# Optimization experiments

Measured on AMD Instinct MI355X. Metric: run time of the kernel, lower is better.

The kernel has to match this reference:

```python
import jax, jax.numpy as jnp
import numpy as np

B, S, D, H, NL, V, E, DFF = 4, 512, 768, 12, 2, 32000, 8, 3072
CF = 1.25
HD = D // H


def setup_inputs() -> dict:
    key = jax.random.key(0)
    ks = jax.random.split(key, 12)
    r = lambda i, shape: jax.random.normal(ks[i], shape, jnp.float32) * 0.02
    return {
        "src": jax.random.randint(ks[0], (B, S), 0, V),
        "src_pad_mask": jnp.zeros((B, S), bool),
        "emb": r(1, (V, D)),
        "qkv_w": r(2, (NL, 3 * D, D)), "qkv_b": jnp.zeros((NL, 3 * D), jnp.float32),
        "out_w": r(3, (NL, D, D)), "out_b": jnp.zeros((NL, D), jnp.float32),
        "wr": r(4, (NL, D, E)),
        "w1": r(5, (NL, E, D, DFF)), "b1": jnp.zeros((NL, E, DFF), jnp.float32),
        "w2": r(6, (NL, E, DFF, D)), "b2": jnp.zeros((NL, E, D), jnp.float32),
        "ln1_g": jnp.ones((NL, D), jnp.float32), "ln1_b": jnp.zeros((NL, D), jnp.float32),
        "ln2_g": jnp.ones((NL, D), jnp.float32), "ln2_b": jnp.zeros((NL, D), jnp.float32),
        "lnf_g": jnp.ones((D,), jnp.float32), "lnf_b": jnp.zeros((D,), jnp.float32),
    }


def layernorm(x, g, b, eps=1e-5):
    mu = jnp.mean(x, -1, keepdims=True)
    var = jnp.mean((x - mu) ** 2, -1, keepdims=True)
    return (x - mu) * jax.lax.rsqrt(var + eps) * g + b


def pos_encoding():
    pos = jnp.arange(S, dtype=jnp.float32)[:, None]
    i = jnp.arange(0, D, 2, dtype=jnp.float32)
    ang = pos * jnp.exp(-(i / D) * jnp.log(jnp.float32(10000.0)))  # [S, D/2]
    pe = jnp.zeros((S, D), jnp.float32)
    pe = pe.at[:, 0::2].set(jnp.sin(ang)).at[:, 1::2].set(jnp.cos(ang))
    return pe


def mha(x, wqkv, bqkv, wo, bo, pad):
    qkv = x @ wqkv.T + bqkv
    q, k, v = jnp.split(qkv, 3, axis=-1)
    q = q.reshape(B, S, H, HD); k = k.reshape(B, S, H, HD); v = v.reshape(B, S, H, HD)
    sc = jnp.einsum('bqhd,bkhd->bhqk', q, k) * (1.0 / float(HD) ** 0.5)
    sc = jnp.where(pad[:, None, None, :], jnp.float32(-1e9), sc)
    at = jax.nn.softmax(sc, -1)
    o = jnp.einsum('bhqk,bkhd->bqhd', at, v).reshape(B, S, D)
    return o @ wo.T + bo


def switch_ffn(x, token_mask, wr, w1, b1, w2, b2):
    # Switch Transformer top-1 routing with capacity drop.
    T = B * S
    cap = int(CF * T / E)
    xf = x.reshape(T, D)
    vm = token_mask.reshape(T).astype(x.dtype)
    logits = xf @ wr                                   # [T, E]
    probs = jax.nn.softmax(logits, -1)
    idx = jnp.argmax(probs, -1)
    gate = jnp.take_along_axis(probs, idx[:, None], -1)[:, 0]
    oh = jax.nn.one_hot(idx, E, dtype=x.dtype) * vm[:, None]      # [T, E]
    pos = jnp.cumsum(oh, axis=0) * oh                  # 1-indexed position in expert
    keep = ((pos > 0) & (pos <= cap)).astype(x.dtype)
    disp = keep[:, :, None] * jax.nn.one_hot((pos - 1).astype(jnp.int32), cap, dtype=x.dtype)  # [T,E,C]
    comb = disp * gate[:, None, None]
    ein = jnp.einsum('tec,td->ecd', disp, xf)          # [E, C, D]
    hid = jax.nn.relu(jnp.einsum('ecd,edf->ecf', ein, w1) + b1[:, None, :])
    eo = jnp.einsum('ecf,efd->ecd', hid, w2) + b2[:, None, :]
    y = jnp.einsum('tec,ecd->td', comb, eo).reshape(B, S, D)
    denom = jnp.maximum(vm.sum(), 1.0)
    me = (probs * vm[:, None]).sum(0) / denom
    ce = oh.sum(0) / denom
    lb = jnp.float32(E) * jnp.sum(me * ce)
    z = jnp.sum((jax.nn.logsumexp(logits, -1) ** 2) * vm) / denom
    return y, lb, z


def forward(src, src_pad_mask, emb, qkv_w, qkv_b, out_w, out_b, wr, w1, b1, w2, b2,
            ln1_g, ln1_b, ln2_g, ln2_b, lnf_g, lnf_b):
    x = emb[src] * jnp.float32(float(D) ** 0.5) + pos_encoding()[None]
    token_mask = ~src_pad_mask
    lbs, zs = [], []
    for l in range(NL):
        xn = layernorm(x, ln1_g[l], ln1_b[l])
        x = x + mha(xn, qkv_w[l], qkv_b[l], out_w[l], out_b[l], src_pad_mask)
        xn = layernorm(x, ln2_g[l], ln2_b[l])
        y, lb, z = switch_ffn(xn, token_mask, wr[l], w1[l], b1[l], w2[l], b2[l])
        x = x + y
        lbs.append(lb); zs.append(z)
    x = layernorm(x, lnf_g, lnf_b)
    return x, jnp.stack(lbs).mean(), jnp.stack(zs).mean()


def reference(src, src_pad_mask, emb, qkv_w, qkv_b, out_w, out_b, wr, w1, b1, w2, b2,
              ln1_g, ln1_b, ln2_g, ln2_b, lnf_g, lnf_b):
    return forward(src, src_pad_mask, emb, qkv_w, qkv_b, out_w, out_b, wr, w1, b1, w2, b2,
                   ln1_g, ln1_b, ln2_g, ln2_b, lnf_g, lnf_b)
```

## Files before the change

### kernel.cpp

```cpp
#include <hip/hip_runtime.h>

#define BB 4
#define SS 512
#define DD 768
#define HH 12
#define NLAYER 2
#define EE 8
#define DFF 3072
#define TT 2048
#define CAP 320
#define HD 64

typedef unsigned short u16;
typedef long long ll;
typedef _Float16 f16x8 __attribute__((ext_vector_type(8)));
typedef float f32x4 __attribute__((ext_vector_type(4)));

union F16U { _Float16 h; u16 u; };

__device__ __forceinline__ void split2h(float v, u16& h0, u16& h1) {
    F16U c0; c0.h = (_Float16)v;
    float r = (v - (float)c0.h) * 4096.0f;
    F16U c1; c1.h = (_Float16)r;
    h0 = c0.u; h1 = c1.u;
}
__device__ __forceinline__ float rec2h(u16 a, u16 b) {
    F16U c0, c1; c0.u = a; c1.u = b;
    return (float)c0.h + (float)c1.h * (1.0f / 4096.0f);
}

#define MFMA16(a, b, c) __builtin_amdgcn_mfma_f32_16x16x32_f16(a, b, c, 0, 0, 0)

struct GemmP {
    const u16* A = nullptr; ll sAp = 0;
    const void* B = nullptr; ll sBp = 0;
    const float* bias = nullptr; ll biasStride = 0;
    void* C = nullptr; ll sCp = 0;
    int M = 0, N = 0, K = 0, lda = 0, ldb = 0, ldc = 0;
    int modA = 1; ll sA1 = 0, sA2 = 0;
    int modB = 1; ll sB1 = 0, sB2 = 0;
    int modC = 1; ll sC1 = 0, sC2 = 0;
    float alpha = 1.f;
    int flags = 0;
    int KS = 1; ll partStride = 0;
    int Jc = 1;
};

#define BK 64
#define PADK 72

template<bool BTRANS, int NS>
__global__ __launch_bounds__(256) void gemm_kernel(GemmP p) {
    __shared__ u16 Al[NS][128][PADK];
    __shared__ u16 Bl[NS][128][PADK];
    const int tid = threadIdx.x;

    int bx, by, bz;
    {
        int gx = gridDim.x, gy = gridDim.y;
        int NBt = gx * gy * gridDim.z;
        int L = blockIdx.x + gx * (blockIdx.y + gy * blockIdx.z);
        int q = NBt >> 3, r = NBt & 7;
        int xcd = L & 7, wi = L >> 3;
        int c = (xcd < r) ? xcd * (q + 1) + wi : r * (q + 1) + (xcd - r) * q + wi;
        int Jc = p.Jc;
        int gxJ = gx * Jc;
        int sj = c / gxJ;
        int t = c - sj * gxJ;
        bx = t / Jc;
        int j = sj * Jc + (t - (t / Jc) * Jc);
        by = j % gy; bz = j / gy;
    }
    const int n0 = bx * 128, m0 = by * 128;
    const int slice = bz % p.KS;
    const int z = bz / p.KS;
    const int kslice = p.K / p.KS;
    const int k0 = slice * kslice;
    const int nkt = kslice >> 6;

    const u16* Ap = p.A + (ll)(z % p.modA) * p.sA1 + (ll)(z / p.modA) * p.sA2 + k0;
    const ll zB = (ll)(z % p.modB) * p.sB1 + (ll)(z / p.modB) * p.sB2;
    const ll zC = (ll)(z % p.modC) * p.sC1 + (ll)(z / p.modC) * p.sC2;
    const u16* Bpu = BTRANS ? ((const u16*)p.B + zB + k0) : nullptr;
    const float* Bpf = BTRANS ? nullptr : ((const float*)p.B + zB);

    const int lane = tid & 63, wid = tid >> 6;
    const int wm = (wid >> 1) * 64, wn = (wid & 1) * 64;
    const int ar = lane & 15, kg = (lane >> 4) * 8;

    f32x4 acc0[4][4] = {};
    f32x4 acc1[4][4] = {};

    uint4 ra[4 * NS];
    uint4 rb[4 * NS];
    float rbf[32];

    auto loadA = [&](int kt) {
        #pragma unroll
        for (int s = 0; s < NS; ++s)
            #pragma unroll
            for (int h = 0; h < 4; ++h) {
                int c = tid + h * 256, row = c >> 3, q = c & 7;
                int gm = m0 + row;
                uint4 v = {0u, 0u, 0u, 0u};
                if (gm < p.M) v = *(const uint4*)(Ap + (ll)s * p.sAp + (size_t)gm * p.lda + kt * BK + q * 8);
                ra[s * 4 + h] = v;
            }
    };
    auto storeA = [&]() {
        #pragma unroll
        for (int s = 0; s < NS; ++s)
            #pragma unroll
            for (int h = 0; h < 4; ++h) {
                int c = tid + h * 256, row = c >> 3, q = c & 7;
                *(uint4*)&Al[s][row][q * 8] = ra[s * 4 + h];
            }
    };
    auto loadB = [&](int kt) {
        if (BTRANS) {
            #pragma unroll
            for (int s = 0; s < NS; ++s)
                #pragma unroll
                for (int h = 0; h < 4; ++h) {
                    int c = tid + h * 256, row = c >> 3, q = c & 7;
                    int gn = n0 + row;
                    uint4 v = {0u, 0u, 0u, 0u};
                    if (gn < p.N) v = *(const uint4*)(Bpu + (ll)s * p.sBp + (size_t)gn * p.ldb + kt * BK + q * 8);
                    rb[s * 4 + h] = v;
                }
        } else {
            int gn = n0 + (tid & 127);
            int kb = (tid >> 7) * 32;
            #pragma unroll
            for (int i = 0; i < 32; ++i) {
                float v = 0.f;
                if (gn < p.N) v = Bpf[(size_t)(k0 + kt * BK + kb + i) * p.ldb + gn];
                rbf[i] = v;
            }
        }
    };
    auto storeB = [&]() {
        if (BTRANS) {
            #pragma unroll
            for (int s = 0; s < NS; ++s)
                #pragma unroll
                for (int h = 0; h < 4; ++h) {
                    int c = tid + h * 256, row = c >> 3, q = c & 7;
                    *(uint4*)&Bl[s][row][q * 8] = rb[s * 4 + h];
                }
        } else {
            int col = tid & 127;
            int kb = (tid >> 7) * 32;
            #pragma unroll
            for (int i = 0; i < 8; ++i) {
                u16 t0[4], t1[4];
                #pragma unroll
                for (int e = 0; e < 4; ++e) split2h(rbf[i * 4 + e], t0[e], t1[e]);
                *(uint2*)&Bl[0][col][kb + i * 4] = *(uint2*)t0;
                if (NS == 2) *(uint2*)&Bl[1][col][kb + i * 4] = *(uint2*)t1;
            }
        }
    };

    loadA(0); loadB(0);
    for (int kt = 0; kt < nkt; ++kt) {
        storeA(); storeB();
        __syncthreads();
        if (kt + 1 < nkt) { loadA(kt + 1); loadB(kt + 1); }
        #pragma unroll
        for (int kt2 = 0; kt2 < 2; ++kt2) {
            f16x8 b0r[4], b1r[4];
            #pragma unroll
            for (int j = 0; j < 4; ++j) {
                b0r[j] = *(const f16x8*)&Bl[0][wn + j * 16 + ar][kt2 * 32 + kg];
                if (NS == 2) b1r[j] = *(const f16x8*)&Bl[1][wn + j * 16 + ar][kt2 * 32 + kg];
            }
            #pragma unroll
            for (int i = 0; i < 4; ++i) {
                f16x8 a0 = *(const f16x8*)&Al[0][wm + i * 16 + ar][kt2 * 32 + kg];
                f16x8 a1;
                if (NS == 2) a1 = *(const f16x8*)&Al[1][wm + i * 16 + ar][kt2 * 32 + kg];
                #pragma unroll
                for (int j = 0; j < 4; ++j) {
                    acc0[i][j] = MFMA16(a0, b0r[j], acc0[i][j]);
                    if (NS == 2) {
                        acc1[i][j] = MFMA16(a0, b1r[j], acc1[i][j]);
                        acc1[i][j] = MFMA16(a1, b0r[j], acc1[i][j]);
                    }
                }
            }
        }
        __syncthreads();
    }

    const bool doPart = (p.flags & 16);
    float* Cpart = doPart ? ((float*)p.C + (ll)slice * p.partStride + zC) : nullptr;
    const float* biasp = (p.flags & 1) ? (p.bias + (ll)z * p.biasStride) : nullptr;
    u16* C0 = (!doPart && (p.flags & 8)) ? ((u16*)p.C + zC) : nullptr;
    u16* C1 = C0 ? (C0 + p.sCp) : nullptr;
    float* Cf = (!doPart && !(p.flags & 8)) ? ((float*)p.C + zC) : nullptr;
    #pragma unroll
    for (int i = 0; i < 4; ++i) {
        #pragma unroll
        for (int j = 0; j < 4; ++j) {
            int gc = n0 + wn + j * 16 + (lane & 15);
            if (gc >= p.N) continue;
            int gr0 = m0 + wm + i * 16 + (lane >> 4) * 4;
            #pragma unroll
            for (int r = 0; r < 4; ++r) {
                int gr = gr0 + r;
                if (gr >= p.M) continue;
                float v = acc0[i][j][r];
                if (NS == 2) v += acc1[i][j][r] * (1.0f / 4096.0f);
                v *= p.alpha;
                size_t off = (size_t)gr * p.ldc + gc;
                if (doPart) { Cpart[off] = v; continue; }
                if (p.flags & 1) v = __fadd_rn(v, biasp[gc]);
                if (p.flags & 2) v = fmaxf(v, 0.f);
                if (p.flags & 8) { u16 h0, h1; split2h(v, h0, h1); C0[off] = h0; C1[off] = h1; }
                else Cf[off] = v;
            }
        }
    }
}

__global__ __launch_bounds__(256) void flash_kernel(
    const u16* __restrict__ qkvp, ll sQp,
    const u16* __restrict__ vTp, ll sVp,
    const unsigned char* __restrict__ pad,
    u16* __restrict__ attnp, ll sOp) {
    __shared__ u16 KV[2][64][72];
    __shared__ u16 Pl[2][4][16][72];

    int L = blockIdx.x;
    int c = (L & 7) * 48 + (L >> 3);
    int bh = c >> 3, qt = c & 7;
    int b = bh / HH, h = bh % HH;
    int lane = threadIdx.x & 63, wv = threadIdx.x >> 6;
    int qbase = b * SS + qt * 64 + wv * 16;

    int spl = threadIdx.x >> 7;
    int srr = threadIdx.x & 127;
    int srow = srr >> 1, shalf = srr & 1;

    f16x8 qf[2][2];
    {
        const u16* qr = qkvp + (size_t)(qbase + (lane & 15)) * (3 * DD) + h * HD + (lane >> 4) * 8;
        #pragma unroll
        for (int kt2 = 0; kt2 < 2; ++kt2)
            #pragma unroll
            for (int pl = 0; pl < 2; ++pl)
                qf[kt2][pl] = *(const f16x8*)(qr + (ll)pl * sQp + kt2 * 32);
    }

    f32x4 S[32];
    #pragma unroll
    for (int kv = 0; kv < 8; ++kv) {
        const u16* gk = qkvp + (size_t)(b * SS + kv * 64 + srow) * (3 * DD) + DD + h * HD + (ll)spl * sQp;
        #pragma unroll
        for (int qq = 0; qq < 4; ++qq) {
            int off = shalf * 32 + qq * 8;
            *(uint4*)&KV[spl][srow][off] = *(const uint4*)(gk + off);
        }
        __syncthreads();
        #pragma unroll
        for (int nf = 0; nf < 4; ++nf) {
            f32x4 a0 = {}, a1 = {};
            #pragma unroll
            for (int kt2 = 0; kt2 < 2; ++kt2) {
                f16x8 b0 = *(const f16x8*)&KV[0][nf * 16 + (lane & 15)][kt2 * 32 + (lane >> 4) * 8];
                f16x8 b1 = *(const f16x8*)&KV[1][nf * 16 + (lane & 15)][kt2 * 32 + (lane >> 4) * 8];
                a0 = MFMA16(qf[kt2][0], b0, a0);
                a1 = MFMA16(qf[kt2][0], b1, a1);
                a1 = MFMA16(qf[kt2][1], b0, a1);
            }
            int col = kv * 64 + nf * 16 + (lane & 15);
            bool msk = pad[b * SS + col] != 0;
            #pragma unroll
            for (int r = 0; r < 4; ++r) {
                float v = (a0[r] + a1[r] * (1.0f / 4096.0f)) * 0.125f;
                S[kv * 4 + nf][r] = msk ? -1e9f : v;
            }
        }
        __syncthreads();
    }

    float mx[4] = {-1e30f, -1e30f, -1e30f, -1e30f}, sm[4] = {0.f, 0.f, 0.f, 0.f}, inv[4];
    #pragma unroll
    for (int f = 0; f < 32; ++f)
        #pragma unroll
        for (int r = 0; r < 4; ++r) mx[r] = fmaxf(mx[r], S[f][r]);
    #pragma unroll
    for (int r = 0; r < 4; ++r) {
        #pragma unroll
        for (int off = 1; off < 16; off <<= 1) mx[r] = fmaxf(mx[r], __shfl_xor(mx[r], off));
    }
    #pragma unroll
    for (int f = 0; f < 32; ++f)
        #pragma unroll
        for (int r = 0; r < 4; ++r) { float e = expf(S[f][r] - mx[r]); S[f][r] = e; sm[r] += e; }
    #pragma unroll
    for (int r = 0; r < 4; ++r) {
        #pragma unroll
        for (int off = 1; off < 16; off <<= 1) sm[r] += __shfl_xor(sm[r], off);
        inv[r] = 1.f / sm[r];
    }

    f32x4 p0[4] = {}, p1[4] = {};
    #pragma unroll
    for (int kv = 0; kv < 8; ++kv) {
        const u16* gv = vTp + (size_t)bh * HD * SS + (size_t)srow * SS + kv * 64 + (ll)spl * sVp;
        #pragma unroll
        for (int qq = 0; qq < 4; ++qq) {
            int off = shalf * 32 + qq * 8;
            *(uint4*)&KV[spl][srow][off] = *(const uint4*)(gv + off);
        }
        #pragma unroll
        for (int nf = 0; nf < 4; ++nf)
            #pragma unroll
            for (int r = 0; r < 4; ++r) {
                float v = S[kv * 4 + nf][r] * inv[r];
                u16 h0, h1; split2h(v, h0, h1);
                Pl[0][wv][(lane >> 4) * 4 + r][nf * 16 + (lane & 15)] = h0;
                Pl[1][wv][(lane >> 4) * 4 + r][nf * 16 + (lane & 15)] = h1;
            }
        __syncthreads();
        f16x8 pa[2][2];
        #pragma unroll
        for (int kt2 = 0; kt2 < 2; ++kt2)
            #pragma unroll
            for (int pl = 0; pl < 2; ++pl)
                pa[kt2][pl] = *(const f16x8*)&Pl[pl][wv][lane & 15][kt2 * 32 + (lane >> 4) * 8];
        #pragma unroll
        for (int df = 0; df < 4; ++df) {
            #pragma unroll
            for (int kt2 = 0; kt2 < 2; ++kt2) {
                f16x8 v0 = *(const f16x8*)&KV[0][df * 16 + (lane & 15)][kt2 * 32 + (lane >> 4) * 8];
                f16x8 v1 = *(const f16x8*)&KV[1][df * 16 + (lane & 15)][kt2 * 32 + (lane >> 4) * 8];
                p0[df] = MFMA16(pa[kt2][0], v0, p0[df]);
                p1[df] = MFMA16(pa[kt2][0], v1, p1[df]);
                p1[df] = MFMA16(pa[kt2][1], v0, p1[df]);
            }
        }
        __syncthreads();
    }

    #pragma unroll
    for (int df = 0; df < 4; ++df)
        #pragma unroll
        for (int r = 0; r < 4; ++r) {
            float v = p0[df][r] + p1[df][r] * (1.0f / 4096.0f);
            int row = qbase + (lane >> 4) * 4 + r;
            int col = h * HD + df * 16 + (lane & 15);
            u16 h0, h1; split2h(v, h0, h1);
            attnp[(size_t)row * DD + col] = h0;
            attnp[(size_t)row * DD + col + sOp] = h1;
        }
}

struct RedP {
    const float* part = nullptr; ll partStride = 0; int KS = 1;
    float* outf = nullptr;
    u16* o0 = nullptr; ll planeStride = 0;
    const float* bias = nullptr; ll biasStride = 0; ll batchElems = 1; int Nc = 1;
    const float* src = nullptr;
    ll total = 0; int mode = 0;
};
__global__ void reduce_kernel(RedP p) {
    ll e0 = ((ll)blockIdx.x * 256 + threadIdx.x) * 4;
    if (e0 >= p.total) return;
    float4 s = *(const float4*)(p.part + e0);
    for (int k = 1; k < p.KS; ++k) {
        float4 t = *(const float4*)(p.part + (ll)k * p.partStride + e0);
        s.x += t.x; s.y += t.y; s.z += t.z; s.w += t.w;
    }
    if (p.mode & 1) {
        ll b = e0 / p.batchElems;
        int d = (int)(e0 % p.Nc);
        float4 bv = *(const float4*)(p.bias + b * p.biasStride + d);
        s.x = __fadd_rn(s.x, bv.x); s.y = __fadd_rn(s.y, bv.y);
        s.z = __fadd_rn(s.z, bv.z); s.w = __fadd_rn(s.w, bv.w);
    }
    if (p.mode & 4) {
        float4 t = *(const float4*)(p.src + e0);
        s.x = __fadd_rn(s.x, t.x); s.y = __fadd_rn(s.y, t.y);
        s.z = __fadd_rn(s.z, t.z); s.w = __fadd_rn(s.w, t.w);
    }
    if (p.mode & 2) { s.x = fmaxf(s.x, 0.f); s.y = fmaxf(s.y, 0.f); s.z = fmaxf(s.z, 0.f); s.w = fmaxf(s.w, 0.f); }
    if (p.mode & 8) {
        u16 t0[4], t1[4];
        float vv[4] = {s.x, s.y, s.z, s.w};
        #pragma unroll
        for (int e = 0; e < 4; ++e) split2h(vv[e], t0[e], t1[e]);
        *(uint2*)(p.o0 + e0) = *(uint2*)t0;
        *(uint2*)(p.o0 + p.planeStride + e0) = *(uint2*)t1;
    } else {
        *(float4*)(p.outf + e0) = s;
    }
}

__global__ void wsplit_kernel(const float* __restrict__ w, u16* __restrict__ p0,
                              ll planeStride, ll total) {
    ll e0 = ((ll)blockIdx.x * 256 + threadIdx.x) * 4;
    if (e0 >= total) return;
    float4 v = *(const float4*)(w + e0);
    u16 t0[4], t1[4];
    float vv[4] = {v.x, v.y, v.z, v.w};
    #pragma unroll
    for (int e = 0; e < 4; ++e) split2h(vv[e], t0[e], t1[e]);
    *(uint2*)(p0 + e0) = *(uint2*)t0;
    *(uint2*)(p0 + planeStride + e0) = *(uint2*)t1;
}

__global__ void vtrans_kernel(const u16* __restrict__ qkvp, ll sQp,
                              u16* __restrict__ vTp, ll sVp) {
    __shared__ float t[32][33];
    int z = blockIdx.z;
    int b = z / HH, h = z % HH;
    int c0 = blockIdx.x * 32, r0 = blockIdx.y * 32;
    int tx = threadIdx.x, ty = threadIdx.y;
    const u16* in = qkvp + (size_t)(b * SS) * (3 * DD) + 2 * DD + h * HD;
    #pragma unroll
    for (int i = 0; i < 32; i += 8) {
        size_t o = (size_t)(r0 + ty + i) * (3 * DD) + c0 + tx;
        t[ty + i][tx] = rec2h(in[o], in[o + sQp]);
    }
    __syncthreads();
    u16* out = vTp + (size_t)z * HD * SS;
    #pragma unroll
    for (int i = 0; i < 32; i += 8) {
        size_t o = (size_t)(c0 + ty + i) * SS + r0 + tx;
        u16 h0, h1; split2h(t[tx][ty + i], h0, h1);
        out[o] = h0; out[o + sVp] = h1;
    }
}

__global__ void pe_kernel(float* __restrict__ pe) {
    int s = blockIdx.x, tid = threadIdx.x;
    const float lg = 9.210340371976184f;
    #pragma unroll
    for (int j = 0; j < 3; ++j) {
        int d = j * 256 + tid;
        int half = d >> 1;
        float fi = (float)(2 * half) / 768.0f;
        float arg = __fmul_rn(-fi, lg);
        float freq = (float)exp((double)arg);
        float ang = __fmul_rn((float)s, freq);
        double da = (double)ang;
        pe[(size_t)s * DD + d] = (d & 1) ? (float)cos(da) : (float)sin(da);
    }
}

__global__ void embed_kernel(const int* __restrict__ src, const float* __restrict__ emb,
                             const float* __restrict__ pe, float* __restrict__ x) {
    int t = blockIdx.x, tid = threadIdx.x;
    int s = t & (SS - 1);
    int tok = src[t];
    const float sq = 27.712812921102035f;
    #pragma unroll
    for (int j = 0; j < 3; ++j) {
        int d = j * 256 + tid;
        float e = emb[(size_t)tok * DD + d];
        x[(size_t)t * DD + d] = __fadd_rn(__fmul_rn(e, sq), pe[(size_t)s * DD + d]);
    }
}

__global__ void ln_kernel(const float* __restrict__ x, const float* __restrict__ g,
                          const float* __restrict__ b, float* __restrict__ outf,
                          u16* __restrict__ op, ll planeStride) {
    int t = blockIdx.x, tid = threadIdx.x;
    const float* xr = x + (size_t)t * DD;
    float v[3], s = 0.f, sq = 0.f;
    #pragma unroll
    for (int j = 0; j < 3; ++j) { v[j] = xr[tid + j * 256]; s += v[j]; sq += v[j] * v[j]; }
    #pragma unroll
    for (int off = 32; off; off >>= 1) { s += __shfl_xor(s, off); sq += __shfl_xor(sq, off); }
    __shared__ float rs[4], rq[4];
    int wid = tid >> 6;
    if ((tid & 63) == 0) { rs[wid] = s; rq[wid] = sq; }
    __syncthreads();
    s = rs[0] + rs[1] + rs[2] + rs[3];
    sq = rq[0] + rq[1] + rq[2] + rq[3];
    float mu = s / 768.0f;
    float var = sq / 768.0f - mu * mu;
    float rstd = rsqrtf(var + 1e-5f);
    #pragma unroll
    for (int j = 0; j < 3; ++j) {
        int d = tid + j * 256;
        float y = __fadd_rn(__fmul_rn(__fmul_rn(v[j] - mu, rstd), g[d]), b[d]);
        if (outf) outf[(size_t)t * DD + d] = y;
        if (op) {
            size_t o = (size_t)t * DD + d;
            u16 h0, h1; split2h(y, h0, h1);
            op[o] = h0; op[o + planeStride] = h1;
        }
    }
}

__global__ void ln2_router_kernel(const float* __restrict__ x, const float* __restrict__ g,
                                  const float* __restrict__ b, const float* __restrict__ wr,
                                  const unsigned char* __restrict__ pad,
                                  u16* __restrict__ op, ll planeStride,
                                  float* __restrict__ probs, float* __restrict__ lsev,
                                  float* __restrict__ gate, int* __restrict__ idx) {
    int t = blockIdx.x, tid = threadIdx.x;
    const float* xr = x + (size_t)t * DD;
    float v[3], s = 0.f, sq = 0.f;
    #pragma unroll
    for (int j = 0; j < 3; ++j) { v[j] = xr[tid + j * 256]; s += v[j]; sq += v[j] * v[j]; }
    #pragma unroll
    for (int off = 32; off; off >>= 1) { s += __shfl_xor(s, off); sq += __shfl_xor(sq, off); }
    __shared__ float rs[4], rq[4];
    __shared__ float ra[4][8];
    int wid = tid >> 6;
    if ((tid & 63) == 0) { rs[wid] = s; rq[wid] = sq; }
    __syncthreads();
    s = rs[0] + rs[1] + rs[2] + rs[3];
    sq = rq[0] + rq[1] + rq[2] + rq[3];
    float mu = s / 768.0f;
    float var = sq / 768.0f - mu * mu;
    float rstd = rsqrtf(var + 1e-5f);
    float a[8] = {0.f, 0.f, 0.f, 0.f, 0.f, 0.f, 0.f, 0.f};
    #pragma unroll
    for (int j = 0; j < 3; ++j) {
        int d = tid + j * 256;
        float y = __fadd_rn(__fmul_rn(__fmul_rn(v[j] - mu, rstd), g[d]), b[d]);
        size_t o = (size_t)t * DD + d;
        u16 h0, h1; split2h(y, h0, h1);
        op[o] = h0; op[o + planeStride] = h1;
        const float* w = wr + (size_t)d * EE;
        #pragma unroll
        for (int e = 0; e < 8; ++e) a[e] += y * w[e];
    }
    #pragma unroll
    for (int off = 32; off; off >>= 1)
        #pragma unroll
        for (int e = 0; e < 8; ++e) a[e] += __shfl_xor(a[e], off);
    if ((tid & 63) == 0)
        #pragma unroll
        for (int e = 0; e < 8; ++e) ra[wid][e] = a[e];
    __syncthreads();
    if (tid == 0) {
        #pragma unroll
        for (int e = 0; e < 8; ++e) a[e] = ra[0][e] + ra[1][e] + ra[2][e] + ra[3][e];
        int vm = (pad[t] == 0);
        float mx = a[0]; int bi = 0;
        #pragma unroll
        for (int e = 1; e < 8; ++e) if (a[e] > mx) { mx = a[e]; bi = e; }
        float ex[8], sum = 0.f;
        #pragma unroll
        for (int e = 0; e < 8; ++e) { ex[e] = expf(a[e] - mx); sum += ex[e]; }
        float inv = 1.f / sum;
        #pragma unroll
        for (int e = 0; e < 8; ++e) probs[(size_t)t * EE + e] = vm ? ex[e] * inv : 0.f;
        lsev[t] = vm ? (mx + logf(sum)) : 0.f;
        gate[t] = ex[bi] * inv;
        idx[t] = vm ? bi : -1;
    }
}

__global__ void route_scan_kernel(const int* __restrict__ idx, const float* __restrict__ probs,
                                  const float* __restrict__ lsev, int* __restrict__ slot,
                                  int* __restrict__ tos, float* __restrict__ acc) {
    int lane = threadIdx.x;
    int base = lane * 32;
    int ev[32];
    int c[8] = {0, 0, 0, 0, 0, 0, 0, 0};
    #pragma unroll
    for (int i = 0; i < 32; ++i) {
        int e = idx[base + i];
        ev[i] = e;
        #pragma unroll
        for (int q = 0; q < 8; ++q) c[q] += (e == q);
    }
    int excl[8], tot[8];
    #pragma unroll
    for (int e = 0; e < 8; ++e) {
        int v = c[e];
        #pragma unroll
        for (int off = 1; off < 64; off <<= 1) {
            int n = __shfl_up(v, off);
            if (lane >= off) v += n;
        }
        excl[e] = v - c[e];
        tot[e] = __shfl(v, 63);
    }
    int r[8];
    #pragma unroll
    for (int e = 0; e < 8; ++e) r[e] = excl[e];
    #pragma unroll
    for (int i = 0; i < 32; ++i) {
        int t = base + i, e = ev[i], s = -1;
        if (e >= 0) {
            int pos = 0;
            #pragma unroll
            for (int q = 0; q < 8; ++q) if (e == q) { r[q]++; pos = r[q]; }
            if (pos <= CAP) { s = e * CAP + pos - 1; tos[s] = t; }
        }
        slot[t] = s;
    }
    float pa[8] = {0.f, 0.f, 0.f, 0.f, 0.f, 0.f, 0.f, 0.f};
    float l2 = 0.f, vld = 0.f;
    #pragma unroll
    for (int i = 0; i < 32; ++i) {
        int t = base + i;
        float lv = lsev[t];
        l2 += lv * lv;
        if (ev[i] >= 0) vld += 1.f;
        #pragma unroll
        for (int e = 0; e < 8; ++e) pa[e] += probs[(size_t)t * EE + e];
    }
    #pragma unroll
    for (int off = 32; off; off >>= 1) {
        #pragma unroll
        for (int e = 0; e < 8; ++e) pa[e] += __shfl_xor(pa[e], off);
        l2 += __shfl_xor(l2, off);
        vld += __shfl_xor(vld, off);
    }
    if (lane == 0) {
        float denom = fmaxf(vld, 1.f);
        float lb = 0.f;
        #pragma unroll
        for (int e = 0; e < 8; ++e) lb += (pa[e] / denom) * ((float)tot[e] / denom);
        lb *= 8.f;
        acc[0] += lb;
        acc[1] += l2 / denom;
    }
}

__global__ void gather_kernel(const int* __restrict__ tos, const u16* __restrict__ xnp,
                              ll sXp, u16* __restrict__ einp, ll sEp) {
    int s = blockIdx.x;
    int tid = threadIdx.x;
    if (tid >= 192) return;
    int pl = tid / 96, q = tid % 96;
    int t = tos[s];
    uint4 v = {0u, 0u, 0u, 0u};
    if (t >= 0) v = *(const uint4*)(xnp + (ll)pl * sXp + (size_t)t * DD + q * 8);
    *(uint4*)(einp + (ll)pl * sEp + (size_t)s * DD + q * 8) = v;
}

__global__ void combine2_kernel(const int* __restrict__ slot, const float* __restrict__ gate,
                                const float* __restrict__ part, ll partStride, int KS,
                                const float* __restrict__ b2, float* __restrict__ x) {
    int t = blockIdx.x, tid = threadIdx.x;
    int s = slot[t];
    if (s < 0) return;
    float gv = gate[t];
    int e = s / CAP;
    #pragma unroll
    for (int j = 0; j < 3; ++j) {
        int d = j * 256 + tid;
        size_t o = (size_t)s * DD + d;
        float v = part[o];
        for (int k = 1; k < KS; ++k) v += part[(ll)k * partStride + o];
        v = __fadd_rn(v, b2[(size_t)e * DD + d]);
        size_t ox = (size_t)t * DD + d;
        x[ox] = __fadd_rn(x[ox], __fmul_rn(gv, v));
    }
}

__global__ void finalize_kernel(const float* __restrict__ acc, float* __restrict__ out) {
    out[(size_t)TT * DD] = acc[0] * (1.f / NLAYER);
    out[(size_t)TT * DD + 1] = acc[1] * (1.f / NLAYER);
}

static inline void run_gemm(bool btrans, int ns, const GemmP& p, dim3 grid, hipStream_t s) {
    if (btrans) {
        gemm_kernel<true, 2><<<grid, 256, 0, s>>>(p);
    } else {
        if (ns == 2) gemm_kernel<false, 2><<<grid, 256, 0, s>>>(p);
        else gemm_kernel<false, 1><<<grid, 256, 0, s>>>(p);
    }
}
static inline void run_reduce(const RedP& r, hipStream_t s) {
    reduce_kernel<<<(int)((r.total / 4 + 255) / 256), 256, 0, s>>>(r);
}

extern "C" void kernel_launch(void* const* d_in, const int* in_sizes, int n_in,
                              void* d_out, int out_size, void* d_ws, size_t ws_size,
                              hipStream_t stream) {
    const int* src = (const int*)d_in[0];
    const unsigned char* pad = (const unsigned char*)d_in[1];
    const float* emb = (const float*)d_in[2];
    const float* qkv_w = (const float*)d_in[3];
    const float* qkv_b = (const float*)d_in[4];
    const float* out_w = (const float*)d_in[5];
    const float* out_b = (const float*)d_in[6];
    const float* wr = (const float*)d_in[7];
    const float* w1 = (const float*)d_in[8];
    const float* b1 = (const float*)d_in[9];
    const float* w2 = (const float*)d_in[10];
    const float* b2 = (const float*)d_in[11];
    const float* ln1_g = (const float*)d_in[12];
    const float* ln1_b = (const float*)d_in[13];
    const float* ln2_g = (const float*)d_in[14];
    const float* ln2_b = (const float*)d_in[15];
    const float* lnf_g = (const float*)d_in[16];
    const float* lnf_b = (const float*)d_in[17];

    char* w = (char*)d_ws;
    size_t off = 0;
    auto alloc = [&](size_t bytes) -> void* {
        void* p = w + off;
        off += (bytes + 255) & ~(size_t)255;
        return p;
    };
    float* x      = (float*)alloc((size_t)TT * DD * 4);
    float* peT    = (float*)alloc((size_t)SS * DD * 4);
    u16*   xnp    = (u16*)  alloc((size_t)2 * TT * DD * 2);
    u16*   qkvp   = (u16*)  alloc((size_t)2 * TT * 3 * DD * 2);
    u16*   vTp    = (u16*)  alloc((size_t)2 * BB * HH * HD * SS * 2);
    u16*   attnp  = (u16*)  alloc((size_t)2 * TT * DD * 2);
    u16*   einp   = (u16*)  alloc((size_t)2 * EE * CAP * DD * 2);
    u16*   hidp   = (u16*)  alloc((size_t)2 * EE * CAP * DFF * 2);
    char*  regB   = (char*) alloc((size_t)2 * TT * 3 * DD * 4);
    u16*   qkvwp  = (u16*)  alloc((size_t)2 * NLAYER * 3 * DD * DD * 2);
    u16*   owp    = (u16*)  alloc((size_t)2 * NLAYER * DD * DD * 2);
    float* probs  = (float*)alloc((size_t)TT * EE * 4);
    float* lsev   = (float*)alloc((size_t)TT * 4);
    float* gate   = (float*)alloc((size_t)TT * 4);
    int*   idx    = (int*)  alloc((size_t)TT * 4);
    int*   slot   = (int*)  alloc((size_t)TT * 4);
    int*   tos    = (int*)  alloc((size_t)EE * CAP * 4);
    float* accb   = (float*)alloc(256);
    if (off > ws_size) return;

    float* qkvpart = (float*)regB;
    float* oppart  = (float*)regB;
    float* ffnpart = (float*)regB;

    hipMemsetAsync(accb, 0, 8, stream);
    pe_kernel<<<SS, 256, 0, stream>>>(peT);
    embed_kernel<<<TT, 256, 0, stream>>>(src, emb, peT, x);

    {
        ll tq = (ll)NLAYER * 3 * DD * DD;
        wsplit_kernel<<<(int)((tq / 4 + 255) / 256), 256, 0, stream>>>(qkv_w, qkvwp, tq, tq);
        ll to = (ll)NLAYER * DD * DD;
        wsplit_kernel<<<(int)((to / 4 + 255) / 256), 256, 0, stream>>>(out_w, owp, to, to);
    }

    for (int l = 0; l < NLAYER; ++l) {
        const int nsF = (l < NLAYER - 1) ? 2 : 1;
        ln_kernel<<<TT, 256, 0, stream>>>(x, ln1_g + l * DD, ln1_b + l * DD, nullptr, xnp, (ll)TT * DD);

        {
            GemmP p;
            p.A = xnp; p.sAp = (ll)TT * DD; p.lda = DD;
            p.B = qkvwp + (size_t)l * 3 * DD * DD; p.sBp = (ll)NLAYER * 3 * DD * DD; p.ldb = DD;
            p.C = qkvpart; p.ldc = 3 * DD;
            p.M = TT; p.N = 3 * DD; p.K = DD;
            p.flags = 16; p.KS = 2; p.partStride = (ll)TT * 3 * DD;
            p.Jc = 4;
            run_gemm(true, 2, p, dim3(18, 16, 2), stream);
        }
        {
            RedP r;
            r.part = qkvpart; r.partStride = (ll)TT * 3 * DD; r.KS = 2;
            r.o0 = qkvp; r.planeStride = (ll)TT * 3 * DD;
            r.bias = qkv_b + (size_t)l * 3 * DD; r.biasStride = 0; r.batchElems = (ll)TT * 3 * DD; r.Nc = 3 * DD;
            r.total = (ll)TT * 3 * DD; r.mode = 1 | 8;
            run_reduce(r, stream);
        }
        vtrans_kernel<<<dim3(HD / 32, SS / 32, BB * HH), dim3(32, 8), 0, stream>>>(
            qkvp, (ll)TT * 3 * DD, vTp, (ll)BB * HH * HD * SS);
        flash_kernel<<<BB * HH * 8, 256, 0, stream>>>(
            qkvp, (ll)TT * 3 * DD, vTp, (ll)BB * HH * HD * SS, pad, attnp, (ll)TT * DD);
        {
            GemmP p;
            p.A = attnp; p.sAp = (ll)TT * DD; p.lda = DD;
            p.B = owp + (size_t)l * DD * DD; p.sBp = (ll)NLAYER * DD * DD; p.ldb = DD;
            p.C = oppart; p.ldc = DD;
            p.M = TT; p.N = DD; p.K = DD;
            p.flags = 16; p.KS = 4; p.partStride = (ll)TT * DD;
            p.Jc = 8;
            run_gemm(true, 2, p, dim3(6, 16, 4), stream);
        }
        {
            RedP r;
            r.part = oppart; r.partStride = (ll)TT * DD; r.KS = 4;
            r.outf = x;
            r.bias = out_b + (size_t)l * DD; r.biasStride = 0; r.batchElems = (ll)TT * DD; r.Nc = DD;
            r.src = x;
            r.total = (ll)TT * DD; r.mode = 1 | 4;
            run_reduce(r, stream);
        }
        ln2_router_kernel<<<TT, 256, 0, stream>>>(x, ln2_g + l * DD, ln2_b + l * DD,
                                                  wr + (size_t)l * DD * EE, pad,
                                                  xnp, (ll)TT * DD, probs, lsev, gate, idx);
        hipMemsetAsync(tos, 0xFF, (size_t)EE * CAP * 4, stream);
        route_scan_kernel<<<1, 64, 0, stream>>>(idx, probs, lsev, slot, tos, accb);
        gather_kernel<<<EE * CAP, 256, 0, stream>>>(tos, xnp, (ll)TT * DD, einp, (ll)EE * CAP * DD);
        {
            GemmP p;
            p.A = einp; p.sAp = (ll)EE * CAP * DD; p.lda = DD;
            p.modA = EE; p.sA1 = (ll)CAP * DD;
            p.B = w1 + (size_t)l * EE * DD * DFF; p.ldb = DFF;
            p.modB = EE; p.sB1 = (ll)DD * DFF;
            p.bias = b1 + (size_t)l * EE * DFF; p.biasStride = DFF;
            p.C = hidp; p.sCp = (ll)EE * CAP * DFF; p.ldc = DFF;
            p.modC = EE; p.sC1 = (ll)CAP * DFF;
            p.M = CAP; p.N = DFF; p.K = DD;
            p.flags = 1 | 2 | 8;
            p.Jc = 3;
            run_gemm(false, nsF, p, dim3(24, 3, EE), stream);
        }
        {
            GemmP p;
            p.A = hidp; p.sAp = (ll)EE * CAP * DFF; p.lda = DFF;
            p.modA = EE; p.sA1 = (ll)CAP * DFF;
            p.B = w2 + (size_t)l * EE * DFF * DD; p.ldb = DD;
            p.modB = EE; p.sB1 = (ll)DFF * DD;
            p.C = ffnpart; p.ldc = DD; p.modC = EE; p.sC1 = (ll)CAP * DD;
            p.M = CAP; p.N = DD; p.K = DFF;
            p.flags = 16; p.KS = 4; p.partStride = (ll)EE * CAP * DD;
            p.Jc = 12;
            run_gemm(false, nsF, p, dim3(6, 3, EE * 4), stream);
        }
        combine2_kernel<<<TT, 256, 0, stream>>>(slot, gate, ffnpart, (ll)EE * CAP * DD, 4,
                                                b2 + (size_t)l * EE * DD, x);
    }
    ln_kernel<<<TT, 256, 0, stream>>>(x, lnf_g, lnf_b, (float*)d_out, nullptr, 0);
    finalize_kernel<<<1, 1, 0, stream>>>(accb, (float*)d_out);
}
```

Before: 786.9 us.

## Pre-transpose and split expert FFN weights into fp16 planes for B-transposed GEMM

Adds a tiled shared-memory transpose kernel that converts each layer's expert w1/w2 weights from fp32 into transposed fp16 hi/lo planes. The expert GEMMs then use the B-transposed fp16 path instead of reading fp32 B in its native layout. The aim is cheaper, contiguous B loads inside the GEMM. In exchange it adds an extra pass over about 150 MB of fp32 weights per layer, plus extra workspace, and the path falls back when the workspace is too small.

New measurement: 841.2 us. 1.07x slower.

```diff
diff --git a/kernel.cpp b/kernel.cpp
--- a/kernel.cpp
+++ b/kernel.cpp
@@ -224,6 +224,33 @@
     }
 }
 
+struct WtP {
+    const float* in; u16* out;
+    int R, C;
+    ll sIn, sOutZ, planeStride;
+    int np;
+};
+__global__ void wtrans_kernel(WtP p) {
+    __shared__ float t[32][33];
+    int z = blockIdx.z;
+    const float* in = p.in + (ll)z * p.sIn;
+    u16* out = p.out + (ll)z * p.sOutZ;
+    int c0 = blockIdx.x * 32, r0 = blockIdx.y * 32;
+    int tx = threadIdx.x, ty = threadIdx.y;
+    #pragma unroll
+    for (int i = 0; i < 32; i += 8)
+        t[ty + i][tx] = in[(size_t)(r0 + ty + i) * p.C + c0 + tx];
+    __syncthreads();
+    #pragma unroll
+    for (int i = 0; i < 32; i += 8) {
+        float v = t[tx][ty + i];
+        size_t o = (size_t)(c0 + ty + i) * p.R + r0 + tx;
+        u16 h0, h1; split2h(v, h0, h1);
+        out[o] = h0;
+        if (p.np == 2) out[o + p.planeStride] = h1;
+    }
+}
+
 __global__ __launch_bounds__(256) void flash_kernel(
     const u16* __restrict__ qkvp, ll sQp,
     const u16* __restrict__ vTp, ll sVp,
@@ -667,7 +694,8 @@
 
 static inline void run_gemm(bool btrans, int ns, const GemmP& p, dim3 grid, hipStream_t s) {
     if (btrans) {
-        gemm_kernel<true, 2><<<grid, 256, 0, s>>>(p);
+        if (ns == 2) gemm_kernel<true, 2><<<grid, 256, 0, s>>>(p);
+        else gemm_kernel<true, 1><<<grid, 256, 0, s>>>(p);
     } else {
         if (ns == 2) gemm_kernel<false, 2><<<grid, 256, 0, s>>>(p);
         else gemm_kernel<false, 1><<<grid, 256, 0, s>>>(p);
@@ -725,6 +753,9 @@
     int*   tos    = (int*)  alloc((size_t)EE * CAP * 4);
     float* accb   = (float*)alloc(256);
     if (off > ws_size) return;
+    u16* w1Tp = (u16*)alloc((size_t)2 * EE * DFF * DD * 2);
+    u16* w2Tp = (u16*)alloc((size_t)2 * EE * DD * DFF * 2);
+    const bool use_tr = (off <= ws_size);
 
     float* qkvpart = (float*)regB;
     float* oppart  = (float*)regB;
@@ -792,31 +823,53 @@
         hipMemsetAsync(tos, 0xFF, (size_t)EE * CAP * 4, stream);
         route_scan_kernel<<<1, 64, 0, stream>>>(idx, probs, lsev, slot, tos, accb);
         gather_kernel<<<EE * CAP, 256, 0, stream>>>(tos, xnp, (ll)TT * DD, einp, (ll)EE * CAP * DD);
+        if (use_tr) {
+            WtP t1; t1.in = w1 + (size_t)l * EE * DD * DFF; t1.out = w1Tp;
+            t1.R = DD; t1.C = DFF; t1.sIn = (ll)DD * DFF; t1.sOutZ = (ll)DFF * DD;
+            t1.planeStride = (ll)EE * DFF * DD; t1.np = nsF;
+            wtrans_kernel<<<dim3(DFF / 32, DD / 32, EE), dim3(32, 8), 0, stream>>>(t1);
+            WtP t2; t2.in = w2 + (size_t)l * EE * DFF * DD; t2.out = w2Tp;
+            t2.R = DFF; t2.C = DD; t2.sIn = (ll)DFF * DD; t2.sOutZ = (ll)DD * DFF;
+            t2.planeStride = (ll)EE * DD * DFF; t2.np = nsF;
+            wtrans_kernel<<<dim3(DD / 32, DFF / 32, EE), dim3(32, 8), 0, stream>>>(t2);
+        }
         {
             GemmP p;
             p.A = einp; p.sAp = (ll)EE * CAP * DD; p.lda = DD;
             p.modA = EE; p.sA1 = (ll)CAP * DD;
-            p.B = w1 + (size_t)l * EE * DD * DFF; p.ldb = DFF;
-            p.modB = EE; p.sB1 = (ll)DD * DFF;
             p.bias = b1 + (size_t)l * EE * DFF; p.biasStride = DFF;
             p.C = hidp; p.sCp = (ll)EE * CAP * DFF; p.ldc = DFF;
             p.modC = EE; p.sC1 = (ll)CAP * DFF;
             p.M = CAP; p.N = DFF; p.K = DD;
             p.flags = 1 | 2 | 8;
             p.Jc = 3;
-            run_gemm(false, nsF, p, dim3(24, 3, EE), stream);
+            if (use_tr) {
+                p.B = w1Tp; p.sBp = (ll)EE * DFF * DD; p.ldb = DD;
+                p.modB = EE; p.sB1 = (ll)DFF * DD;
+                run_gemm(true, nsF, p, dim3(24, 3, EE), stream);
+            } else {
+                p.B = w1 + (size_t)l * EE * DD * DFF; p.ldb = DFF;
+                p.modB = EE; p.sB1 = (ll)DD * DFF;
+                run_gemm(false, nsF, p, dim3(24, 3, EE), stream);
+            }
         }
         {
             GemmP p;
             p.A = hidp; p.sAp = (ll)EE * CAP * DFF; p.lda = DFF;
             p.modA = EE; p.sA1 = (ll)CAP * DFF;
-            p.B = w2 + (size_t)l * EE * DFF * DD; p.ldb = DD;
-            p.modB = EE; p.sB1 = (ll)DFF * DD;
             p.C = ffnpart; p.ldc = DD; p.modC = EE; p.sC1 = (ll)CAP * DD;
             p.M = CAP; p.N = DD; p.K = DFF;
             p.flags = 16; p.KS = 4; p.partStride = (ll)EE * CAP * DD;
             p.Jc = 12;
-            run_gemm(false, nsF, p, dim3(6, 3, EE * 4), stream);
+            if (use_tr) {
+                p.B = w2Tp; p.sBp = (ll)EE * DD * DFF; p.ldb = DFF;
+                p.modB = EE; p.sB1 = (ll)DD * DFF;
+                run_gemm(true, nsF, p, dim3(6, 3, EE * 4), stream);
+            } else {
+                p.B = w2 + (size_t)l * EE * DFF * DD; p.ldb = DD;
+                p.modB = EE; p.sB1 = (ll)DFF * DD;
+                run_gemm(false, nsF, p, dim3(6, 3, EE * 4), stream);
+            }
         }
         combine2_kernel<<<TT, 256, 0, stream>>>(slot, gate, ffnpart, (ll)EE * CAP * DD, 4,
                                                 b2 + (size_t)l * EE * DD, x);
```

## Fuse expert token gather into FFN1 GEMM and split-K FFN1 with reduce

Applied to the files above, without the earlier changes.

The separate gather kernel that copied routed tokens into a per-expert buffer is removed. The first expert GEMM now reads A rows indirectly through the token-to-slot table, with rows resolved once per block. FFN1 also switches from a direct-epilogue GEMM with bias/activation to a 2-way split-K GEMM writing fp32 partials, followed by a reduce kernel that applies bias and activation and writes the hidden activations. This saves one launch and one buffer round trip but adds fp32 partial traffic and an extra reduce pass. The workspace region is enlarged to hold the partials.

After: 843.2 us. +7.1%, slower.

```diff
diff --git a/kernel.cpp b/kernel.cpp
--- a/kernel.cpp
+++ b/kernel.cpp
@@ -44,6 +44,7 @@
     int flags = 0;
     int KS = 1; ll partStride = 0;
     int Jc = 1;
+    const int* tosA = nullptr;
 };
 
 #define BK 64
@@ -95,15 +96,32 @@
     uint4 rb[4 * NS];
     float rbf[32];
 
+    int tosr[4];
+    if (p.tosA) {
+        #pragma unroll
+        for (int h = 0; h < 4; ++h) {
+            int c = tid + h * 256, row = c >> 3;
+            int gm = m0 + row;
+            tosr[h] = (gm < p.M) ? p.tosA[(ll)z * CAP + gm] : -1;
+        }
+    }
+
     auto loadA = [&](int kt) {
         #pragma unroll
         for (int s = 0; s < NS; ++s)
             #pragma unroll
             for (int h = 0; h < 4; ++h) {
                 int c = tid + h * 256, row = c >> 3, q = c & 7;
-                int gm = m0 + row;
                 uint4 v = {0u, 0u, 0u, 0u};
-                if (gm < p.M) v = *(const uint4*)(Ap + (ll)s * p.sAp + (size_t)gm * p.lda + kt * BK + q * 8);
+                if (p.tosA) {
+                    int t = tosr[h];
+                    if (t >= 0)
+                        v = *(const uint4*)(p.A + (ll)s * p.sAp + (size_t)t * p.lda + k0 + kt * BK + q * 8);
+                } else {
+                    int gm = m0 + row;
+                    if (gm < p.M)
+                        v = *(const uint4*)(Ap + (ll)s * p.sAp + (size_t)gm * p.lda + kt * BK + q * 8);
+                }
                 ra[s * 4 + h] = v;
             }
     };
@@ -628,18 +646,6 @@
     }
 }
 
-__global__ void gather_kernel(const int* __restrict__ tos, const u16* __restrict__ xnp,
-                              ll sXp, u16* __restrict__ einp, ll sEp) {
-    int s = blockIdx.x;
-    int tid = threadIdx.x;
-    if (tid >= 192) return;
-    int pl = tid / 96, q = tid % 96;
-    int t = tos[s];
-    uint4 v = {0u, 0u, 0u, 0u};
-    if (t >= 0) v = *(const uint4*)(xnp + (ll)pl * sXp + (size_t)t * DD + q * 8);
-    *(uint4*)(einp + (ll)pl * sEp + (size_t)s * DD + q * 8) = v;
-}
-
 __global__ void combine2_kernel(const int* __restrict__ slot, const float* __restrict__ gate,
                                 const float* __restrict__ part, ll partStride, int KS,
                                 const float* __restrict__ b2, float* __restrict__ x) {
@@ -667,7 +673,8 @@
 
 static inline void run_gemm(bool btrans, int ns, const GemmP& p, dim3 grid, hipStream_t s) {
     if (btrans) {
-        gemm_kernel<true, 2><<<grid, 256, 0, s>>>(p);
+        if (ns == 2) gemm_kernel<true, 2><<<grid, 256, 0, s>>>(p);
+        else gemm_kernel<true, 1><<<grid, 256, 0, s>>>(p);
     } else {
         if (ns == 2) gemm_kernel<false, 2><<<grid, 256, 0, s>>>(p);
         else gemm_kernel<false, 1><<<grid, 256, 0, s>>>(p);
@@ -712,9 +719,8 @@
     u16*   qkvp   = (u16*)  alloc((size_t)2 * TT * 3 * DD * 2);
     u16*   vTp    = (u16*)  alloc((size_t)2 * BB * HH * HD * SS * 2);
     u16*   attnp  = (u16*)  alloc((size_t)2 * TT * DD * 2);
-    u16*   einp   = (u16*)  alloc((size_t)2 * EE * CAP * DD * 2);
     u16*   hidp   = (u16*)  alloc((size_t)2 * EE * CAP * DFF * 2);
-    char*  regB   = (char*) alloc((size_t)2 * TT * 3 * DD * 4);
+    char*  regB   = (char*) alloc((size_t)2 * EE * CAP * DFF * 4);
     u16*   qkvwp  = (u16*)  alloc((size_t)2 * NLAYER * 3 * DD * DD * 2);
     u16*   owp    = (u16*)  alloc((size_t)2 * NLAYER * DD * DD * 2);
     float* probs  = (float*)alloc((size_t)TT * EE * 4);
@@ -726,9 +732,10 @@
     float* accb   = (float*)alloc(256);
     if (off > ws_size) return;
 
-    float* qkvpart = (float*)regB;
-    float* oppart  = (float*)regB;
-    float* ffnpart = (float*)regB;
+    float* qkvpart  = (float*)regB;
+    float* oppart   = (float*)regB;
+    float* ffn1part = (float*)regB;
+    float* ffn2part = (float*)regB;
 
     hipMemsetAsync(accb, 0, 8, stream);
     pe_kernel<<<SS, 256, 0, stream>>>(peT);
@@ -791,20 +798,25 @@
                                                   xnp, (ll)TT * DD, probs, lsev, gate, idx);
         hipMemsetAsync(tos, 0xFF, (size_t)EE * CAP * 4, stream);
         route_scan_kernel<<<1, 64, 0, stream>>>(idx, probs, lsev, slot, tos, accb);
-        gather_kernel<<<EE * CAP, 256, 0, stream>>>(tos, xnp, (ll)TT * DD, einp, (ll)EE * CAP * DD);
         {
             GemmP p;
-            p.A = einp; p.sAp = (ll)EE * CAP * DD; p.lda = DD;
-            p.modA = EE; p.sA1 = (ll)CAP * DD;
+            p.A = xnp; p.sAp = (ll)TT * DD; p.lda = DD;
+            p.tosA = tos;
             p.B = w1 + (size_t)l * EE * DD * DFF; p.ldb = DFF;
             p.modB = EE; p.sB1 = (ll)DD * DFF;
-            p.bias = b1 + (size_t)l * EE * DFF; p.biasStride = DFF;
-            p.C = hidp; p.sCp = (ll)EE * CAP * DFF; p.ldc = DFF;
-            p.modC = EE; p.sC1 = (ll)CAP * DFF;
+            p.C = ffn1part; p.ldc = DFF; p.modC = EE; p.sC1 = (ll)CAP * DFF;
             p.M = CAP; p.N = DFF; p.K = DD;
-            p.flags = 1 | 2 | 8;
-            p.Jc = 3;
-            run_gemm(false, nsF, p, dim3(24, 3, EE), stream);
+            p.flags = 16; p.KS = 2; p.partStride = (ll)EE * CAP * DFF;
+            p.Jc = 6;
+            run_gemm(false, nsF, p, dim3(24, 3, EE * 2), stream);
+        }
+        {
+            RedP r;
+            r.part = ffn1part; r.partStride = (ll)EE * CAP * DFF; r.KS = 2;
+            r.o0 = hidp; r.planeStride = (ll)EE * CAP * DFF;
+            r.bias = b1 + (size_t)l * EE * DFF; r.biasStride = DFF; r.batchElems = (ll)CAP * DFF; r.Nc = DFF;
+            r.total = (ll)EE * CAP * DFF; r.mode = 1 | 2 | 8;
+            run_reduce(r, stream);
         }
         {
             GemmP p;
@@ -812,13 +824,13 @@
             p.modA = EE; p.sA1 = (ll)CAP * DFF;
             p.B = w2 + (size_t)l * EE * DFF * DD; p.ldb = DD;
             p.modB = EE; p.sB1 = (ll)DFF * DD;
-            p.C = ffnpart; p.ldc = DD; p.modC = EE; p.sC1 = (ll)CAP * DD;
+            p.C = ffn2part; p.ldc = DD; p.modC = EE; p.sC1 = (ll)CAP * DD;
             p.M = CAP; p.N = DD; p.K = DFF;
             p.flags = 16; p.KS = 4; p.partStride = (ll)EE * CAP * DD;
             p.Jc = 12;
             run_gemm(false, nsF, p, dim3(6, 3, EE * 4), stream);
         }
-        combine2_kernel<<<TT, 256, 0, stream>>>(slot, gate, ffnpart, (ll)EE * CAP * DD, 4,
+        combine2_kernel<<<TT, 256, 0, stream>>>(slot, gate, ffn2part, (ll)EE * CAP * DD, 4,
                                                 b2 + (size_t)l * EE * DD, x);
     }
     ln_kernel<<<TT, 256, 0, stream>>>(x, lnf_g, lnf_b, (float*)d_out, nullptr, 0);
```
